# Kernel tuning notes

Measured on AMD Instinct MI355X. Metric: run time of the kernel, lower is better.

The kernel has to match this reference:

```python
import jax, jax.numpy as jnp
import numpy as np

EPS = 1e-8

def setup_inputs() -> dict:
    key = jax.random.key(0)
    ks = jax.random.split(key, 8)
    B, D, N, F = 8192, 1024, 2048, 8
    d2 = D // 2
    # integer-valued data (IDF acts on integers)
    x = jnp.round(jax.random.normal(ks[0], (B, D), jnp.float32) * 5.0)
    s1 = 1.0 / np.sqrt(d2)
    s2 = 1.0 / np.sqrt(N)
    return {
        "x": x,
        "W1": jax.random.normal(ks[1], (F, d2, N), jnp.float32) * s1,
        "b1": jax.random.normal(ks[2], (F, N), jnp.float32) * 0.01,
        "W2": jax.random.normal(ks[3], (F, N, N), jnp.float32) * s2,
        "b2": jax.random.normal(ks[4], (F, N), jnp.float32) * 0.01,
        "W3": jax.random.normal(ks[5], (F, N, d2), jnp.float32) * s2,
        "b3": jax.random.normal(ks[6], (F, d2), jnp.float32) * 0.01,
        "mean": jnp.zeros((1, D), jnp.float32),
        "log_scale": jnp.ones((1, D), jnp.float32),
    }

def _st_round(v):
    # straight-through round: forward round, identity gradient
    return v + jax.lax.stop_gradient(jnp.round(v) - v)

def _flow(x, W1, b1, W2, b2, W3, b3):
    d2 = x.shape[1] // 2
    def step(z, p):
        w1, bb1, w2, bb2, w3, bb3 = p
        xa, xb = z[:, :d2], z[:, d2:]
        h = jax.nn.leaky_relu(xa @ w1 + bb1)          # [B, N]
        h = jax.nn.leaky_relu(h @ w2 + bb2)           # [B, N]
        t = h @ w3 + bb3                               # [B, d2]
        yb = xb + _st_round(t)
        z = jnp.concatenate([xa, yb], axis=1)[:, ::-1]  # coupling + flip permute
        return z, None
    z, _ = jax.lax.scan(step, x, (W1, b1, W2, b2, W3, b3))
    return z

def reference(x, W1, b1, W2, b2, W3, b3, mean, log_scale):
    z = _flow(x, W1, b1, W2, b2, W3, b3)
    # discretized logistic log-prior: log(sig((z+.5-m)/s) - sig((z-.5-m)/s))
    scale = jnp.exp(log_scale)
    la = jax.nn.log_sigmoid((z + 0.5 - mean) / scale)
    lb = jax.nn.log_sigmoid((z - 0.5 - mean) / scale)
    log_p = la + jnp.log(1.0 - jnp.exp(lb - la) + EPS)  # log_min_exp
    return -log_p.sum(axis=1).mean()  # reduction='avg'
```

## Files before the change

### kernel.cpp

```cpp
#include <hip/hip_runtime.h>
#include <hip/hip_bf16.h>
#include <cmath>


typedef __bf16 bf16_t;
typedef bf16_t bf16x4 __attribute__((ext_vector_type(4)));
typedef bf16_t bf16x8 __attribute__((ext_vector_type(8)));
typedef float floatx4 __attribute__((ext_vector_type(4)));

#define BQ 8192
#define DD 1024
#define D2 512
#define NH 2048
#define NF 8

__device__ __forceinline__ void gload_lds16(const void* g, void* l) {
    __builtin_amdgcn_global_load_lds(
        (__attribute__((address_space(1))) void*)g,
        (__attribute__((address_space(3))) void*)l, 16, 0, 0);
}

__global__ __launch_bounds__(256)
void transpose_bf16(const float* __restrict__ W, bf16_t* __restrict__ Wt,
                    int K, int N) {
    __shared__ float tile[32][33];
    size_t fo = (size_t)blockIdx.z * K * N;
    int n0 = blockIdx.x * 32, k0 = blockIdx.y * 32;
    int tx = threadIdx.x & 31, ty = threadIdx.x >> 5;
    for (int i = 0; i < 4; i++)
        tile[ty + i*8][tx] = W[fo + (size_t)(k0 + ty + i*8) * N + n0 + tx];
    __syncthreads();
    for (int i = 0; i < 4; i++)
        Wt[fo + (size_t)(n0 + ty + i*8) * K + k0 + tx] = (bf16_t)tile[tx][ty + i*8];
}

__global__ __launch_bounds__(256)
void init_SA(const float4* __restrict__ x, float4* __restrict__ S,
             bf16_t* __restrict__ Ab) {
    int idx = blockIdx.x * blockDim.x + threadIdx.x;
    float4 v = x[idx];
    S[idx] = v;
    int col4 = idx & (DD/4 - 1);
    if (col4 < D2/4) {
        int m = idx >> 8;
        bf16x4 p;
        p[0] = (bf16_t)v.x; p[1] = (bf16_t)v.y;
        p[2] = (bf16_t)v.z; p[3] = (bf16_t)v.w;
        ((bf16x4*)Ab)[(size_t)m * (D2/4) + col4] = p;
    }
}

template<int MODE, int K, int TM, int TN, int MINW>
__global__ __launch_bounds__(256, MINW)
void gemm_kernel(const bf16_t* __restrict__ A, const bf16_t* __restrict__ Bt,
                 const float* __restrict__ bias,
                 bf16_t* __restrict__ Cout, float* __restrict__ S,
                 bf16_t* __restrict__ Abn,
                 int N, int rflag)
{
    constexpr int IM   = TM / 32;
    constexpr int JN   = TN / 32;
    constexpr int NA   = TM / 64;
    constexpr int NBD  = TN / 64;
    constexpr int NDMA = NA + NBD;
    constexpr int T    = K / 32;
    static_assert((T - 1) % 3 == 0, "pipeline triple-unroll needs (T-1)%3==0");
    static_assert(JN % 4 == 0, "bff processed in groups of 4");

    __shared__ __align__(16) bf16_t As[3][TM * 32];
    __shared__ __align__(16) bf16_t Bs[3][TN * 32];

    const int tid  = threadIdx.x;
    const int lane = tid & 63;
    const int wave = tid >> 6;
    const int wm   = wave >> 1;
    const int wn   = wave & 1;
    const int m0   = blockIdx.y * TM;
    const int n0   = blockIdx.x * TN;

    const int srow = tid >> 2;
    const int sq   = ((tid & 3) ^ ((srow >> 1) & 3)) * 8;
    const bf16_t* agp = A  + (size_t)(m0 + srow) * K + sq;
    const bf16_t* bgp = Bt + (size_t)(n0 + srow) * K + sq;

    floatx4 acc[IM][JN];
#pragma unroll
    for (int i = 0; i < IM; i++)
#pragma unroll
        for (int j = 0; j < JN; j++)
            acc[i][j] = (floatx4){0.f, 0.f, 0.f, 0.f};

    const int fr  = lane & 15;
    const int fp8 = ((lane >> 4) ^ ((lane >> 1) & 3)) * 8;

#define ISSUE_TILE(NB)                                                       \
    {                                                                        \
        _Pragma("unroll")                                                    \
        for (int u = 0; u < NA; u++)                                         \
            gload_lds16(agp + (size_t)(u*64) * K, &As[NB][u*2048 + tid*8]);  \
        _Pragma("unroll")                                                    \
        for (int u = 0; u < NBD; u++)                                        \
            gload_lds16(bgp + (size_t)(u*64) * K, &Bs[NB][u*2048 + tid*8]);  \
        agp += 32; bgp += 32;                                                \
    }

#define COMPUTE(CB)                                                          \
    {                                                                        \
        bf16x8 af[IM];                                                       \
        _Pragma("unroll")                                                    \
        for (int i = 0; i < IM; i++)                                         \
            af[i] = *(const bf16x8*)&As[CB][(wm*(TM/2) + i*16 + fr)*32 + fp8];\
        _Pragma("unroll")                                                    \
        for (int g2 = 0; g2 < JN/4; g2++) {                                  \
            bf16x8 bff[4];                                                   \
            _Pragma("unroll")                                                \
            for (int j = 0; j < 4; j++)                                      \
                bff[j] = *(const bf16x8*)                                    \
                    &Bs[CB][(wn*(TN/2) + (g2*4+j)*16 + fr)*32 + fp8];        \
            _Pragma("unroll")                                                \
            for (int i = 0; i < IM; i++)                                     \
                _Pragma("unroll")                                            \
                for (int j = 0; j < 4; j++)                                  \
                    acc[i][g2*4+j] = __builtin_amdgcn_mfma_f32_16x16x32_bf16(\
                                    af[i], bff[j], acc[i][g2*4+j], 0, 0, 0); \
        }                                                                    \
    }

#define PIPE_STEP(NB, CB)                                                    \
    {                                                                        \
        ISSUE_TILE(NB);                                                      \
        __builtin_amdgcn_s_waitcnt(0x0F70 | NDMA);     \
        __builtin_amdgcn_s_barrier();                                        \
        COMPUTE(CB);                                                         \
    }

    ISSUE_TILE(0);

#pragma unroll 1
    for (int g = 0; g < (T - 1) / 3; ++g) {
        PIPE_STEP(1, 0);
        PIPE_STEP(2, 1);
        PIPE_STEP(0, 2);
    }
    __builtin_amdgcn_s_waitcnt(0x0F70);
    __builtin_amdgcn_s_barrier();
    COMPUTE(0);

#undef PIPE_STEP
#undef COMPUTE
#undef ISSUE_TILE

    const int ccol  = lane & 15;
    const int crow4 = (lane >> 4) * 4;
#pragma unroll
    for (int j = 0; j < JN; j++) {
        int col = n0 + wn*(TN/2) + j*16 + ccol;
        float bj = bias[col];
        if (MODE == 0) {
#pragma unroll
            for (int i = 0; i < IM; i++) {
#pragma unroll
                for (int r = 0; r < 4; r++) {
                    int row = m0 + wm*(TM/2) + i*16 + crow4 + r;
                    float v = acc[i][j][r] + bj;
                    v = v >= 0.f ? v : 0.01f * v;
                    Cout[(size_t)row * N + col] = (bf16_t)v;
                }
            }
        } else {
            int slot = rflag ? (511 - col) : (512 + col);
            int aj   = 511 - col;
#pragma unroll
            for (int i = 0; i < IM; i++) {
#pragma unroll
                for (int r = 0; r < 4; r++) {
                    int row = m0 + wm*(TM/2) + i*16 + crow4 + r;
                    float t = acc[i][j][r] + bj;
                    float nv = S[(size_t)row * DD + slot] + rintf(t);
                    S[(size_t)row * DD + slot] = nv;
                    Abn[(size_t)row * D2 + aj] = (bf16_t)nv;
                }
            }
        }
    }
}

template<int K, int TM, int TN>
__global__ __launch_bounds__(256, 2)
void gemm2b_kernel(const bf16_t* __restrict__ A, const bf16_t* __restrict__ Bt,
                   const float* __restrict__ bias, bf16_t* __restrict__ Cout,
                   int N)
{
    constexpr int IM   = TM / 32;
    constexpr int JN   = TN / 32;
    constexpr int NA   = TM / 64;
    constexpr int NBD  = TN / 64;
    constexpr int T    = K / 32;
    static_assert(T >= 2, "need >=2 K-tiles");
    static_assert(JN % 4 == 0, "bff processed in groups of 4");

    __shared__ __align__(16) bf16_t As[2][TM * 32];
    __shared__ __align__(16) bf16_t Bs[2][TN * 32];

    const int tid  = threadIdx.x;
    const int lane = tid & 63;
    const int wave = tid >> 6;
    const int wm   = wave >> 1;
    const int wn   = wave & 1;
    const int m0   = blockIdx.y * TM;
    const int n0   = blockIdx.x * TN;

    const int srow = tid >> 2;
    const int sq   = ((tid & 3) ^ ((srow >> 1) & 3)) * 8;
    const bf16_t* agp = A  + (size_t)(m0 + srow) * K + sq;
    const bf16_t* bgp = Bt + (size_t)(n0 + srow) * K + sq;

    floatx4 acc[IM][JN];
#pragma unroll
    for (int i = 0; i < IM; i++)
#pragma unroll
        for (int j = 0; j < JN; j++)
            acc[i][j] = (floatx4){0.f, 0.f, 0.f, 0.f};

    const int fr  = lane & 15;
    const int fp8 = ((lane >> 4) ^ ((lane >> 1) & 3)) * 8;

#define ISSUE_TILE(NB)                                                       \
    {                                                                        \
        _Pragma("unroll")                                                    \
        for (int u = 0; u < NA; u++)                                         \
            gload_lds16(agp + (size_t)(u*64) * K, &As[NB][u*2048 + tid*8]);  \
        _Pragma("unroll")                                                    \
        for (int u = 0; u < NBD; u++)                                        \
            gload_lds16(bgp + (size_t)(u*64) * K, &Bs[NB][u*2048 + tid*8]);  \
        agp += 32; bgp += 32;                                                \
    }

#define COMPUTE(CB)                                                          \
    {                                                                        \
        bf16x8 af[IM];                                                       \
        _Pragma("unroll")                                                    \
        for (int i = 0; i < IM; i++)                                         \
            af[i] = *(const bf16x8*)&As[CB][(wm*(TM/2) + i*16 + fr)*32 + fp8];\
        _Pragma("unroll")                                                    \
        for (int g2 = 0; g2 < JN/4; g2++) {                                  \
            bf16x8 bff[4];                                                   \
            _Pragma("unroll")                                                \
            for (int j = 0; j < 4; j++)                                      \
                bff[j] = *(const bf16x8*)                                    \
                    &Bs[CB][(wn*(TN/2) + (g2*4+j)*16 + fr)*32 + fp8];        \
            _Pragma("unroll")                                                \
            for (int i = 0; i < IM; i++)                                     \
                _Pragma("unroll")                                            \
                for (int j = 0; j < 4; j++)                                  \
                    acc[i][g2*4+j] = __builtin_amdgcn_mfma_f32_16x16x32_bf16(\
                                    af[i], bff[j], acc[i][g2*4+j], 0, 0, 0); \
        }                                                                    \
    }

    ISSUE_TILE(0);
    __builtin_amdgcn_s_waitcnt(0x0F70);
    __builtin_amdgcn_s_barrier();

#pragma unroll 1
    for (int tau = 0; tau < T; ++tau) {
        if (tau + 1 < T) ISSUE_TILE((tau + 1) & 1);
        COMPUTE(tau & 1);
        if (tau + 1 < T) {
            __builtin_amdgcn_s_waitcnt(0x0F70);
            __builtin_amdgcn_s_barrier();
        }
    }

#undef COMPUTE
#undef ISSUE_TILE

    const int ccol  = lane & 15;
    const int crow4 = (lane >> 4) * 4;
#pragma unroll
    for (int j = 0; j < JN; j++) {
        int col = n0 + wn*(TN/2) + j*16 + ccol;
        float bj = bias[col];
#pragma unroll
        for (int i = 0; i < IM; i++) {
#pragma unroll
            for (int r = 0; r < 4; r++) {
                int row = m0 + wm*(TM/2) + i*16 + crow4 + r;
                float v = acc[i][j][r] + bj;
                v = v >= 0.f ? v : 0.01f * v;
                Cout[(size_t)row * N + col] = (bf16_t)v;
            }
        }
    }
}

__global__ __launch_bounds__(256)
void reduce_nll(const float* __restrict__ S, const float* __restrict__ mean,
                const float* __restrict__ log_scale, float* __restrict__ out)
{
    float local = 0.f;
    const int total = BQ * DD;
    for (int idx = blockIdx.x * blockDim.x + threadIdx.x; idx < total;
         idx += gridDim.x * blockDim.x) {
        int j = idx & (DD - 1);
        float z  = S[idx];
        float mu = mean[j];
        float sc = expf(log_scale[j]);
        float ua = (z + 0.5f - mu) / sc;
        float ub = (z - 0.5f - mu) / sc;
        float la = fminf(ua, 0.f) - log1pf(expf(-fabsf(ua)));
        float lb = fminf(ub, 0.f) - log1pf(expf(-fabsf(ub)));
        float lp = la + logf(1.0f - expf(lb - la) + 1e-8f);
        local += lp;
    }
    __shared__ float red[256];
    red[threadIdx.x] = local;
    __syncthreads();
    for (int s = 128; s > 0; s >>= 1) {
        if (threadIdx.x < s) red[threadIdx.x] += red[threadIdx.x + s];
        __syncthreads();
    }
    if (threadIdx.x == 0) atomicAdd(out, -red[0] * (1.0f / (float)BQ));
}

extern "C" void kernel_launch(void* const* d_in, const int* in_sizes, int n_in,
                              void* d_out, int out_size, void* d_ws, size_t ws_size,
                              hipStream_t stream)
{
    const float* x   = (const float*)d_in[0];
    const float* W1  = (const float*)d_in[1];
    const float* b1  = (const float*)d_in[2];
    const float* W2  = (const float*)d_in[3];
    const float* b2  = (const float*)d_in[4];
    const float* W3  = (const float*)d_in[5];
    const float* b3  = (const float*)d_in[6];
    const float* mean = (const float*)d_in[7];
    const float* lsc  = (const float*)d_in[8];

    char* ws = (char*)d_ws;
    bf16_t* Wt1 = (bf16_t*)ws; ws += (size_t)NF * NH * D2 * 2;
    bf16_t* Wt2 = (bf16_t*)ws; ws += (size_t)NF * NH * NH * 2;
    bf16_t* Wt3 = (bf16_t*)ws; ws += (size_t)NF * D2 * NH * 2;
    float*  S   = (float*)ws;  ws += (size_t)BQ * DD * 4;
    bf16_t* Ab  = (bf16_t*)ws; ws += (size_t)BQ * D2 * 2;
    bf16_t* H1  = (bf16_t*)ws; ws += (size_t)BQ * NH * 2;
    bf16_t* H2  = (bf16_t*)ws;

    hipMemsetAsync(d_out, 0, sizeof(float), stream);

    dim3 blk(256);
    transpose_bf16<<<dim3(NH/32, D2/32, NF), blk, 0, stream>>>(W1, Wt1, D2, NH);
    transpose_bf16<<<dim3(NH/32, NH/32, NF), blk, 0, stream>>>(W2, Wt2, NH, NH);
    transpose_bf16<<<dim3(D2/32, NH/32, NF), blk, 0, stream>>>(W3, Wt3, NH, D2);

    init_SA<<<BQ * DD / 4 / 256, blk, 0, stream>>>((const float4*)x, (float4*)S, Ab);

    for (int f = 0; f < NF; ++f) {
        int r = f & 1;
        gemm2b_kernel<D2, 128, 128><<<dim3(NH/128, BQ/128), blk, 0, stream>>>(
            Ab, Wt1 + (size_t)f * NH * D2, b1 + (size_t)f * NH, H1, NH);
        gemm2b_kernel<NH, 128, 128><<<dim3(NH/128, BQ/128), blk, 0, stream>>>(
            H1, Wt2 + (size_t)f * NH * NH, b2 + (size_t)f * NH, H2, NH);
        gemm_kernel<1, NH, 64, 128, 3><<<dim3(D2/128, BQ/64), blk, 0, stream>>>(
            H2, Wt3 + (size_t)f * D2 * NH, b3 + (size_t)f * D2, nullptr, S,
            Ab, D2, r);
    }

    reduce_nll<<<2048, blk, 0, stream>>>(S, mean, lsc, (float*)d_out);
}
```

Before: 1.587 ms.

## Use 128x256 triple-buffered tiles for first GEMMs and split-K the third

The first two GEMMs of each flow step now run on the triple-buffered gemm_kernel with 128x256 tiles instead of the double-buffered 128x128 kernel. The goal is more data reuse per LDS tile and better latency hiding. The third GEMM is split four ways along K with 128x128 tiles, which gives more blocks to fill the CUs. Its partial sums are written as bf16 into the H1 buffer, and a separate epilogue kernel adds the partials and the bias, rounds, and updates S and Ab. This adds extra kernel launches and global traffic for the partials. Storing partials in bf16 may also change the rounded coupling values slightly.

After: 1.536 ms. 3.2% less time.

```diff
diff --git a/kernel.cpp b/kernel.cpp
--- a/kernel.cpp
+++ b/kernel.cpp
@@ -54,9 +54,7 @@
 __global__ __launch_bounds__(256, MINW)
 void gemm_kernel(const bf16_t* __restrict__ A, const bf16_t* __restrict__ Bt,
                  const float* __restrict__ bias,
-                 bf16_t* __restrict__ Cout, float* __restrict__ S,
-                 bf16_t* __restrict__ Abn,
-                 int N, int rflag)
+                 bf16_t* __restrict__ Cout, int N)
 {
     constexpr int IM   = TM / 32;
     constexpr int JN   = TN / 32;
@@ -156,46 +154,30 @@
     for (int j = 0; j < JN; j++) {
         int col = n0 + wn*(TN/2) + j*16 + ccol;
         float bj = bias[col];
-        if (MODE == 0) {
-#pragma unroll
-            for (int i = 0; i < IM; i++) {
-#pragma unroll
-                for (int r = 0; r < 4; r++) {
-                    int row = m0 + wm*(TM/2) + i*16 + crow4 + r;
-                    float v = acc[i][j][r] + bj;
-                    v = v >= 0.f ? v : 0.01f * v;
-                    Cout[(size_t)row * N + col] = (bf16_t)v;
-                }
-            }
-        } else {
-            int slot = rflag ? (511 - col) : (512 + col);
-            int aj   = 511 - col;
-#pragma unroll
-            for (int i = 0; i < IM; i++) {
-#pragma unroll
-                for (int r = 0; r < 4; r++) {
-                    int row = m0 + wm*(TM/2) + i*16 + crow4 + r;
-                    float t = acc[i][j][r] + bj;
-                    float nv = S[(size_t)row * DD + slot] + rintf(t);
-                    S[(size_t)row * DD + slot] = nv;
-                    Abn[(size_t)row * D2 + aj] = (bf16_t)nv;
-                }
+#pragma unroll
+        for (int i = 0; i < IM; i++) {
+#pragma unroll
+            for (int r = 0; r < 4; r++) {
+                int row = m0 + wm*(TM/2) + i*16 + crow4 + r;
+                float v = acc[i][j][r] + bj;
+                v = v >= 0.f ? v : 0.01f * v;
+                Cout[(size_t)row * N + col] = (bf16_t)v;
             }
         }
     }
 }
 
-template<int K, int TM, int TN>
+template<int KSTR, int KDEP>
 __global__ __launch_bounds__(256, 2)
-void gemm2b_kernel(const bf16_t* __restrict__ A, const bf16_t* __restrict__ Bt,
-                   const float* __restrict__ bias, bf16_t* __restrict__ Cout,
-                   int N)
-{
-    constexpr int IM   = TM / 32;
-    constexpr int JN   = TN / 32;
-    constexpr int NA   = TM / 64;
-    constexpr int NBD  = TN / 64;
-    constexpr int T    = K / 32;
+void gemm3s_kernel(const bf16_t* __restrict__ A, const bf16_t* __restrict__ Bt,
+                   bf16_t* __restrict__ Pout)
+{
+    constexpr int TM = 128, TN = 128;
+    constexpr int IM = TM / 32;
+    constexpr int JN = TN / 32;
+    constexpr int NA = TM / 64;
+    constexpr int NBD = TN / 64;
+    constexpr int T  = KDEP / 32;
     static_assert(T >= 2, "need >=2 K-tiles");
     static_assert(JN % 4 == 0, "bff processed in groups of 4");
 
@@ -209,11 +191,12 @@
     const int wn   = wave & 1;
     const int m0   = blockIdx.y * TM;
     const int n0   = blockIdx.x * TN;
+    const int koff = blockIdx.z * KDEP;
 
     const int srow = tid >> 2;
     const int sq   = ((tid & 3) ^ ((srow >> 1) & 3)) * 8;
-    const bf16_t* agp = A  + (size_t)(m0 + srow) * K + sq;
-    const bf16_t* bgp = Bt + (size_t)(n0 + srow) * K + sq;
+    const bf16_t* agp = A  + (size_t)(m0 + srow) * KSTR + koff + sq;
+    const bf16_t* bgp = Bt + (size_t)(n0 + srow) * KSTR + koff + sq;
 
     floatx4 acc[IM][JN];
 #pragma unroll
@@ -225,18 +208,18 @@
     const int fr  = lane & 15;
     const int fp8 = ((lane >> 4) ^ ((lane >> 1) & 3)) * 8;
 
-#define ISSUE_TILE(NB)                                                       \
+#define ISSUE_TILE3(NB)                                                      \
     {                                                                        \
         _Pragma("unroll")                                                    \
         for (int u = 0; u < NA; u++)                                         \
-            gload_lds16(agp + (size_t)(u*64) * K, &As[NB][u*2048 + tid*8]);  \
+            gload_lds16(agp + (size_t)(u*64) * KSTR, &As[NB][u*2048 + tid*8]);\
         _Pragma("unroll")                                                    \
         for (int u = 0; u < NBD; u++)                                        \
-            gload_lds16(bgp + (size_t)(u*64) * K, &Bs[NB][u*2048 + tid*8]);  \
+            gload_lds16(bgp + (size_t)(u*64) * KSTR, &Bs[NB][u*2048 + tid*8]);\
         agp += 32; bgp += 32;                                                \
     }
 
-#define COMPUTE(CB)                                                          \
+#define COMPUTE3(CB)                                                         \
     {                                                                        \
         bf16x8 af[IM];                                                       \
         _Pragma("unroll")                                                    \
@@ -258,39 +241,64 @@
         }                                                                    \
     }
 
-    ISSUE_TILE(0);
+    ISSUE_TILE3(0);
     __builtin_amdgcn_s_waitcnt(0x0F70);
     __builtin_amdgcn_s_barrier();
 
 #pragma unroll 1
     for (int tau = 0; tau < T; ++tau) {
-        if (tau + 1 < T) ISSUE_TILE((tau + 1) & 1);
-        COMPUTE(tau & 1);
+        if (tau + 1 < T) ISSUE_TILE3((tau + 1) & 1);
+        COMPUTE3(tau & 1);
         if (tau + 1 < T) {
             __builtin_amdgcn_s_waitcnt(0x0F70);
             __builtin_amdgcn_s_barrier();
         }
     }
 
-#undef COMPUTE
-#undef ISSUE_TILE
-
+#undef COMPUTE3
+#undef ISSUE_TILE3
+
+    bf16_t* P = Pout + (size_t)blockIdx.z * BQ * D2;
     const int ccol  = lane & 15;
     const int crow4 = (lane >> 4) * 4;
 #pragma unroll
     for (int j = 0; j < JN; j++) {
         int col = n0 + wn*(TN/2) + j*16 + ccol;
-        float bj = bias[col];
 #pragma unroll
         for (int i = 0; i < IM; i++) {
 #pragma unroll
             for (int r = 0; r < 4; r++) {
                 int row = m0 + wm*(TM/2) + i*16 + crow4 + r;
-                float v = acc[i][j][r] + bj;
-                v = v >= 0.f ? v : 0.01f * v;
-                Cout[(size_t)row * N + col] = (bf16_t)v;
+                P[(size_t)row * D2 + col] = (bf16_t)acc[i][j][r];
             }
         }
+    }
+}
+
+__global__ __launch_bounds__(256)
+void g3_epilogue(const bf16_t* __restrict__ P, const float* __restrict__ b3,
+                 float* __restrict__ S, bf16_t* __restrict__ Ab, int rflag)
+{
+    int idx = blockIdx.x * blockDim.x + threadIdx.x;
+    int row = idx >> 7;
+    int c4  = (idx & 127) * 4;
+    bf16x4 p0 = ((const bf16x4*)(P                        ))[idx];
+    bf16x4 p1 = ((const bf16x4*)(P + (size_t)1*BQ*D2))[idx];
+    bf16x4 p2 = ((const bf16x4*)(P + (size_t)2*BQ*D2))[idx];
+    bf16x4 p3 = ((const bf16x4*)(P + (size_t)3*BQ*D2))[idx];
+    float4 bb = ((const float4*)b3)[idx & 127];
+    float tv[4];
+#pragma unroll
+    for (int e = 0; e < 4; ++e)
+        tv[e] = (float)p0[e] + (float)p1[e] + (float)p2[e] + (float)p3[e]
+              + ((const float*)&bb)[e];
+#pragma unroll
+    for (int e = 0; e < 4; ++e) {
+        int col  = c4 + e;
+        int slot = rflag ? (511 - col) : (512 + col);
+        float nv = S[(size_t)row * DD + slot] + rintf(tv[e]);
+        S[(size_t)row * DD + slot] = nv;
+        Ab[(size_t)row * D2 + (511 - col)] = (bf16_t)nv;
     }
 }
 
@@ -345,6 +353,7 @@
     bf16_t* Ab  = (bf16_t*)ws; ws += (size_t)BQ * D2 * 2;
     bf16_t* H1  = (bf16_t*)ws; ws += (size_t)BQ * NH * 2;
     bf16_t* H2  = (bf16_t*)ws;
+    bf16_t* P3  = H1;
 
     hipMemsetAsync(d_out, 0, sizeof(float), stream);
 
@@ -357,13 +366,14 @@
 
     for (int f = 0; f < NF; ++f) {
         int r = f & 1;
-        gemm2b_kernel<D2, 128, 128><<<dim3(NH/128, BQ/128), blk, 0, stream>>>(
+        gemm_kernel<0, D2, 128, 256, 2><<<dim3(NH/256, BQ/128), blk, 0, stream>>>(
             Ab, Wt1 + (size_t)f * NH * D2, b1 + (size_t)f * NH, H1, NH);
-        gemm2b_kernel<NH, 128, 128><<<dim3(NH/128, BQ/128), blk, 0, stream>>>(
+        gemm_kernel<0, NH, 128, 256, 2><<<dim3(NH/256, BQ/128), blk, 0, stream>>>(
             H1, Wt2 + (size_t)f * NH * NH, b2 + (size_t)f * NH, H2, NH);
-        gemm_kernel<1, NH, 64, 128, 3><<<dim3(D2/128, BQ/64), blk, 0, stream>>>(
-            H2, Wt3 + (size_t)f * D2 * NH, b3 + (size_t)f * D2, nullptr, S,
-            Ab, D2, r);
+        gemm3s_kernel<NH, 512><<<dim3(D2/128, BQ/128, 4), blk, 0, stream>>>(
+            H2, Wt3 + (size_t)f * D2 * NH, P3);
+        g3_epilogue<<<BQ * D2 / 4 / 256, blk, 0, stream>>>(
+            P3, b3 + (size_t)f * D2, S, Ab, r);
     }
 
     reduce_nll<<<2048, blk, 0, stream>>>(S, mean, lsc, (float*)d_out);
```
